# Kernel tuning notes

Measured on AMD Instinct MI355X. Metric: run time of the kernel, lower is better.

The kernel has to match this reference:

```python
import jax, jax.numpy as jnp
import numpy as np

B, S, D, H = 4, 1024, 1024, 16
HD = D // H          # head space dim = 64
FF = 4 * D           # ffn hidden = 4096
EPS = 1e-6

# ---- Lorentz manifold helpers (curvature k=1: -t^2 + |s|^2 = -1) ----

def to_manifold(space):
    t = jnp.sqrt(jnp.sum(space * space, -1, keepdims=True) + 1.0)
    return jnp.concatenate([t, space], -1)

def l_inner(x, y):
    return -x[..., 0] * y[..., 0] + jnp.sum(x[..., 1:] * y[..., 1:], -1)

def project(z):
    # renormalize onto hyperboloid: z / sqrt(|<z,z>_L|)   (Lorentz midpoint / LResNet)
    d = jnp.sqrt(jnp.clip(-l_inner(z, z), EPS))
    return z / d[..., None]

def hyp_layernorm(x, g, b):
    s = x[..., 1:]
    mu = jnp.mean(s, -1, keepdims=True)
    var = jnp.var(s, -1, keepdims=True)
    s = (s - mu) * jax.lax.rsqrt(var + 1e-5) * g + b
    return to_manifold(s)

def apply_rope(xs, cos, sin):
    # xs [B,S,H,HD]; cos/sin [S,HD//2]; freqs broadcast as [1,S,1,HD//2]
    x2 = xs.reshape(*xs.shape[:-1], HD // 2, 2)
    c = cos[None, :, None, :]
    s = sin[None, :, None, :]
    xr = x2[..., 0] * c - x2[..., 1] * s
    xi = x2[..., 0] * s + x2[..., 1] * c
    return jnp.stack([xr, xi], -1).reshape(xs.shape)


def setup_inputs() -> dict:
    key = jax.random.key(0)
    ks = jax.random.split(key, 8)
    def w(k, shape, fan_in):
        return jax.random.normal(k, shape, jnp.float32) / np.sqrt(fan_in).astype(np.float32)
    x = to_manifold(0.5 * jax.random.normal(ks[0], (B, S, D), jnp.float32))
    pos = jnp.arange(S, dtype=jnp.float32)[:, None]
    inv = 1.0 / (10000.0 ** (jnp.arange(0, HD, 2, dtype=jnp.float32) / HD))
    ang = pos * inv[None, :]
    return {
        'x': x,
        'rope_cos': jnp.cos(ang), 'rope_sin': jnp.sin(ang),
        'norm1_g': jnp.ones((D,), jnp.float32), 'norm1_b': jnp.zeros((D,), jnp.float32),
        'Wq': w(ks[1], (H, D + 1, HD), D + 1), 'bq': jnp.zeros((H, HD), jnp.float32),
        'Wk': w(ks[2], (H, D + 1, HD), D + 1), 'bk': jnp.zeros((H, HD), jnp.float32),
        'Wv': w(ks[3], (H, D + 1, HD), D + 1), 'bv': jnp.zeros((H, HD), jnp.float32),
        'attn_scale': jnp.asarray(np.sqrt(HD), jnp.float32),
        'attn_bias': jnp.zeros((), jnp.float32),
        'Wo': w(ks[4], (H * (HD + 1), D), H * (HD + 1)), 'bo': jnp.zeros((D,), jnp.float32),
        'w_res1': jnp.asarray(1.0, jnp.float32),
        'norm2_g': jnp.ones((D,), jnp.float32), 'norm2_b': jnp.zeros((D,), jnp.float32),
        'W1': w(ks[5], (D + 1, FF), D + 1), 'b1': jnp.zeros((FF,), jnp.float32),
        'W2': w(ks[6], (FF + 1, D), FF + 1), 'b2': jnp.zeros((D,), jnp.float32),
        'w_res2': jnp.asarray(1.0, jnp.float32),
    }


def reference(x, rope_cos, rope_sin, norm1_g, norm1_b, Wq, bq, Wk, bk, Wv, bv,
              attn_scale, attn_bias, Wo, bo, w_res1, norm2_g, norm2_b,
              W1, b1, W2, b2, w_res2):
    # ---- pre-norm ----
    xn = hyp_layernorm(x, norm1_g, norm1_b)
    # ---- per-head Lorentz linear (space part), inline RoPE on q/k ----
    qs = jnp.einsum('bsd,hde->bshe', xn, Wq) + bq          # [B,S,H,HD]
    ksp = jnp.einsum('bsd,hde->bshe', xn, Wk) + bk
    vsp = jnp.einsum('bsd,hde->bshe', xn, Wv) + bv
    qs = apply_rope(qs, rope_cos, rope_sin)
    ksp = apply_rope(ksp, rope_cos, rope_sin)
    # hyperbolic normalization of q/k: unit space norm, time recomputed
    qs = qs * jax.lax.rsqrt(jnp.sum(qs * qs, -1, keepdims=True) + EPS)
    ksp = ksp * jax.lax.rsqrt(jnp.sum(ksp * ksp, -1, keepdims=True) + EPS)
    q = to_manifold(qs)                                    # [B,S,H,HD+1]
    k = to_manifold(ksp)
    v = to_manifold(vsp)
    # ---- curvature-aware scores: 2 + 2 <q,k>_L (neg sq Lorentz distance) ----
    sgn = jnp.concatenate([-jnp.ones((1,), q.dtype), jnp.ones((HD,), q.dtype)])
    cin = jnp.einsum('bshe,bthe->bhst', q * sgn, k)        # Minkowski inner [B,H,S,S]
    att = (2.0 + 2.0 * cin) / attn_scale + attn_bias
    P = jax.nn.softmax(att, axis=-1)
    # ---- Lorentz midpoint aggregation of values ----
    m = jnp.einsum('bhst,bthe->bshe', P, v)
    m = project(m)                                         # back onto hyperboloid
    # ---- heads concat + output Lorentz linear ----
    cat = m.reshape(B, S, H * (HD + 1))
    attn_out = to_manifold(cat @ Wo + bo)
    # ---- LResNet residual 1 ----
    x = project(x + w_res1 * attn_out)
    # ---- Lorentz FFN ----
    h = hyp_layernorm(x, norm2_g, norm2_b)
    h = to_manifold(jax.nn.gelu(h @ W1 + b1))
    mlp = to_manifold(h @ W2 + b2)
    # ---- LResNet residual 2 ----
    x = project(x + w_res2 * mlp)
    return x
```

## Files before the change

kernel.cpp:

```cpp
#include <hip/hip_runtime.h>
#include <hip/hip_bf16.h>

typedef __hip_bfloat16 bf16;
typedef __attribute__((ext_vector_type(8))) short short8;
typedef __attribute__((ext_vector_type(4))) float f32x4;

#define B_  4
#define S_  1024
#define H_  16
#define R_  4096
#define LD_ 1088

#define MBL 1048576L
#define OFF_WQKVT (0L)
#define OFF_WOT   (6684672L)
#define OFF_X2    (0L)
#define OFF_W1T   (9L*MBL)
#define OFF_W2T   (18L*MBL)
#define OFF_BIAS  (26L*MBL)
#define OFF_XNB   (27L*MBL + MBL/2)
#define OFF_MCAT  OFF_XNB
#define OFF_HBUF  OFF_XNB
#define OFF_QPS   (36L*MBL)
#define OFF_ARAW  OFF_QPS
#define OFF_KPS   (44L*MBL)
#define OFF_VT    (52L*MBL)
#define OFF_QT    (62L*MBL)
#define OFF_KT    (62L*MBL + 262144L)
#define OFF_HHBIG (44L*MBL)
#define OFF_MLPB  (76L*MBL)
#define OFF_HHC   (36L*MBL)
#define OFF_MLPF  (44L*MBL)
#define BQKV 0
#define BOF  16384
#define B1F  32768
#define B2F  65536
#define W2R0 81920
#define RCF  98304
#define RSNF 262144
#define SCLF 409600
#define TACC 425984
#define FLAG 458752

__device__ __forceinline__ bf16  f2bf(float v) { return __float2bfloat16(v); }
__device__ __forceinline__ float bf2f(bf16 v)  { return __bfloat162float(v); }
__device__ __forceinline__ unsigned short bf2s(float v) {
  return __builtin_bit_cast(unsigned short, __float2bfloat16(v));
}
__device__ __forceinline__ float ldu(const void* p, long i, int isbf) {
  return isbf ? bf2f(((const bf16*)p)[i]) : ((const float*)p)[i];
}
__device__ __forceinline__ void stu(void* p, long i, float v, int isbf) {
  if (isbf) ((bf16*)p)[i] = f2bf(v);
  else      ((float*)p)[i] = v;
}
__device__ __forceinline__ float gelu_f(float v) {
  const float u = 0.7978845608028654f * (v + 0.044715f * v * v * v);
  const float e = __expf(fminf(2.f * u, 80.f));
  return 0.5f * v * (1.f + (e - 1.f) / (e + 1.f));
}
__device__ __forceinline__ float bfu_lo(unsigned u) {
  return __builtin_bit_cast(float, u << 16);
}
__device__ __forceinline__ float bfu_hi(unsigned u) {
  return __builtin_bit_cast(float, u & 0xFFFF0000u);
}

__device__ __forceinline__ void gload16(const bf16* g, short* l) {
  __builtin_amdgcn_global_load_lds(
      (const __attribute__((address_space(1))) unsigned int*)g,
      (__attribute__((address_space(3))) unsigned int*)l, 16, 0, 0);
}

__global__ void detect_kernel(const unsigned* __restrict__ g, int* __restrict__ flag) {
  if (threadIdx.x == 0) flag[0] = (g[0] == 0x3F803F80u) ? 1 : 0;
}

__global__ __launch_bounds__(256) void zero16_kernel(uint4* __restrict__ p, int n16) {
  int i = blockIdx.x * 256 + threadIdx.x;
  if (i < n16) p[i] = uint4{0, 0, 0, 0};
}

__device__ __forceinline__ float bred_f(float v, float* sh) {
#pragma unroll
  for (int o = 32; o; o >>= 1) v += __shfl_xor(v, o);
  __syncthreads();
  if ((threadIdx.x & 63) == 0) sh[threadIdx.x >> 6] = v;
  __syncthreads();
  return sh[0] + sh[1] + sh[2] + sh[3];
}
__device__ __forceinline__ double bred_d(double v, double* sh) {
#pragma unroll
  for (int o = 32; o; o >>= 1) v += __shfl_xor(v, o);
  __syncthreads();
  if ((threadIdx.x & 63) == 0) sh[threadIdx.x >> 6] = v;
  __syncthreads();
  return sh[0] + sh[1] + sh[2] + sh[3];
}

__global__ __launch_bounds__(256) void mega_prep(
    const void* x, const void* rc, const void* rsn, const void* n1g, const void* n1b,
    const void* Wq, const void* bq, const void* Wk, const void* bk,
    const void* Wv, const void* bv, const void* scl, const void* ab,
    const void* Wo, const void* bo, const void* wr1,
    const void* W1, const void* b1, const void* W2, const void* b2, const void* wr2,
    char* bias_base, bf16* __restrict__ wqkvT, bf16* __restrict__ woT,
    bf16* __restrict__ w1T, bf16* __restrict__ w2T, bf16* __restrict__ xnb,
    const int* __restrict__ flag) {
  const int isbf = flag[0];
  __shared__ float tl[64][65];
  const int tid = threadIdx.x;
  int bid = blockIdx.x;
  if (bid < 297) {
    int i = bid * 256 + tid;
    float* bqkvf = (float*)(bias_base + BQKV);
    if (i < 1024)        { bqkvf[i] = ldu(bq, i, isbf); return; }
    if (i < 2048)        { bqkvf[i] = ldu(bk, i - 1024, isbf); return; }
    if (i < 3072)        { bqkvf[i] = ldu(bv, i - 2048, isbf); return; }
    if (i < 4096)        { ((float*)(bias_base + BOF))[i - 3072] = ldu(bo, i - 3072, isbf); return; }
    if (i < 8192)        { ((float*)(bias_base + B1F))[i - 4096] = ldu(b1, i - 4096, isbf); return; }
    if (i < 9216)        { ((float*)(bias_base + B2F))[i - 8192] = ldu(b2, i - 8192, isbf); return; }
    if (i < 10240)       { ((float*)(bias_base + W2R0))[i - 9216] = ldu(W2, i - 9216, isbf); return; }
    if (i < 10240+32768) { ((float*)(bias_base + RCF))[i - 10240] = ldu(rc, i - 10240, isbf); return; }
    if (i < 10240+65536) { ((float*)(bias_base + RSNF))[i - 43008] = ldu(rsn, i - 43008, isbf); return; }
    if (i == 75776)      { ((float*)(bias_base + SCLF))[0] = ldu(scl, 0, isbf); return; }
    if (i == 75777)      { ((float*)(bias_base + SCLF))[1] = ldu(ab, 0, isbf); return; }
    if (i == 75778)      { ((float*)(bias_base + SCLF))[2] = ldu(wr1, 0, isbf); return; }
    if (i == 75779)      { ((float*)(bias_base + SCLF))[3] = ldu(wr2, 0, isbf); return; }
    return;
  }
  bid -= 297;
  const int tx = tid & 63, tg = tid >> 6;
  if (bid < 816) {
    int k0 = (bid % 17) * 64, z = bid / 17;
    int mode = z >> 4, h = z & 15;
    const void* src = (mode == 0) ? Wq : (mode == 1) ? Wk : Wv;
    const long soff = (long)h * 1025 * 64;
    int base_n = mode * 1024 + h * 64;
    for (int i = tg; i < 64; i += 4) {
      int k = k0 + i;
      tl[i][tx] = (k < 1025) ? ldu(src, soff + (long)k * 64 + tx, isbf) : 0.f;
    }
    __syncthreads();
    for (int i = tg; i < 64; i += 4) {
      int k = k0 + tx;
      if (k < LD_) wqkvT[(long)(base_n + i) * LD_ + k] = f2bf(tl[tx][i]);
    }
    return;
  }
  bid -= 816;
  if (bid < 272) {
    int k0 = (bid % 17) * 64, n0 = (bid / 17) * 64;
    for (int i = tg; i < 64; i += 4) {
      int kp = k0 + i;
      float v = 0.f;
      if (kp < 1056) {
        int h = kp / 66, e = kp - h * 66;
        if (e < 65) v = ldu(Wo, (long)(h * 65 + e) * 1024 + n0 + tx, isbf);
      }
      tl[i][tx] = v;
    }
    __syncthreads();
    for (int i = tg; i < 64; i += 4) {
      int kp = k0 + tx;
      if (kp < LD_) woT[(long)(n0 + i) * LD_ + kp] = f2bf(tl[tx][i]);
    }
    return;
  }
  bid -= 272;
  if (bid < 1088) {
    int k0 = (bid % 17) * 64, n0 = (bid / 17) * 64;
    for (int i = tg; i < 64; i += 4) {
      int k = k0 + i;
      tl[i][tx] = (k < 1025) ? ldu(W1, (long)k * 4096 + n0 + tx, isbf) : 0.f;
    }
    __syncthreads();
    for (int i = tg; i < 64; i += 4) {
      int k = k0 + tx;
      if (k < LD_) w1T[(long)(n0 + i) * LD_ + k] = f2bf(tl[tx][i]);
    }
    return;
  }
  bid -= 1088;
  if (bid < 1024) {
    int k0 = (bid % 64) * 64, n0 = (bid / 64) * 64;
    for (int i = tg; i < 64; i += 4) {
      int k = k0 + i;
      tl[i][tx] = ldu(W2, 1024 + (long)k * 1024 + n0 + tx, isbf);
    }
    __syncthreads();
    for (int i = tg; i < 64; i += 4) {
      int k = k0 + tx;
      w2T[(long)(n0 + i) * 4096 + k] = f2bf(tl[tx][i]);
    }
    return;
  }
  bid -= 1024;
  {
    float* red = &tl[0][0];
    const long base = (long)bid * 1025;
    const long obase = (long)bid * LD_;
    float v[4];
#pragma unroll
    for (int i = 0; i < 4; i++) v[i] = ldu(x, base + 1 + tid * 4 + i, isbf);
    float s = 0.f, s2 = 0.f;
#pragma unroll
    for (int i = 0; i < 4; i++) { s += v[i]; s2 += v[i] * v[i]; }
    s  = bred_f(s,  red);
    s2 = bred_f(s2, red);
    const float mu  = s * (1.f / 1024.f);
    const float var = s2 * (1.f / 1024.f) - mu * mu;
    const float rs  = rsqrtf(var + 1e-5f);
    float n[4], ns = 0.f;
#pragma unroll
    for (int i = 0; i < 4; i++) {
      const int e = tid * 4 + i;
      n[i] = (v[i] - mu) * rs * ldu(n1g, e, isbf) + ldu(n1b, e, isbf);
      ns += n[i] * n[i];
    }
    ns = bred_f(ns, red);
    if (tid == 0) xnb[obase] = f2bf(sqrtf(ns + 1.f));
#pragma unroll
    for (int i = 0; i < 4; i++) xnb[obase + 1 + tid * 4 + i] = f2bf(n[i]);
    if (tid < 63) xnb[obase + 1025 + tid] = f2bf(0.f);
  }
}

template <int EPI, bool SS>
__global__ __launch_bounds__(256) void mfma_gemm(const bf16* __restrict__ A, int lda,
                                                 const bf16* __restrict__ Bw, int ldb, int K,
                                                 const float* __restrict__ bias,
                                                 void* __restrict__ Cv, int ldc, int accf,
                                                 float* __restrict__ tacc) {
  __shared__ __align__(16) short As[2][128 * 32];
  __shared__ __align__(16) short Bs[2][64 * 32];
  const int tid = threadIdx.x, lane = tid & 63, wv = tid >> 6;
  const int quad = lane >> 4, q15 = lane & 15;
  const int wave_m = wv & 1, wave_n = wv >> 1;
  const int n0 = blockIdx.x * 64, m0 = blockIdx.y * 128;
  const int sa0 = wv * 128 + lane, sa1 = sa0 + 64;
  const int ra0 = sa0 >> 2, ca0 = (sa0 & 3) ^ (ra0 & 3);
  const int ra1 = sa1 >> 2, ca1 = (sa1 & 3) ^ (ra1 & 3);
  const int rb = tid >> 2, cb = (tid & 3) ^ (rb & 3);
  const int kswz = (quad ^ (q15 & 3)) * 8;
  const bf16* pa0 = A + (long)(m0 + ra0) * lda + ca0 * 8;
  const bf16* pa1 = A + (long)(m0 + ra1) * lda + ca1 * 8;
  const bf16* pb  = Bw + (long)(n0 + rb) * ldb + cb * 8;
  f32x4 acc[4][2] = {};
  for (int k0 = 0; k0 < K; k0 += 64) {
#pragma unroll
    for (int p = 0; p < 2; p++) {
      gload16(pa0 + p * 32, As[p] + sa0 * 8);
      gload16(pa1 + p * 32, As[p] + sa1 * 8);
      gload16(pb + p * 32, Bs[p] + tid * 8);
    }
    pa0 += 64; pa1 += 64; pb += 64;
    __syncthreads();
#pragma unroll
    for (int p = 0; p < 2; p++) {
      short8 af[4], bfr[2];
#pragma unroll
      for (int i = 0; i < 4; i++)
        af[i] = *(const short8*)(As[p] + (wave_m * 64 + i * 16 + q15) * 32 + kswz);
#pragma unroll
      for (int i = 0; i < 2; i++)
        bfr[i] = *(const short8*)(Bs[p] + (wave_n * 32 + i * 16 + q15) * 32 + kswz);
#pragma unroll
      for (int mi = 0; mi < 4; mi++)
#pragma unroll
        for (int ni = 0; ni < 2; ni++)
          acc[mi][ni] = __builtin_amdgcn_mfma_f32_16x16x32_bf16(af[mi], bfr[ni], acc[mi][ni], 0, 0, 0);
    }
    __syncthreads();
  }
#pragma unroll
  for (int mi = 0; mi < 4; mi++) {
#pragma unroll
    for (int r = 0; r < 4; r++) {
      const int m = m0 + wave_m * 64 + mi * 16 + quad * 4 + r;
      float s2 = 0.f;
#pragma unroll
      for (int ni = 0; ni < 2; ni++) {
        const int n = n0 + wave_n * 32 + ni * 16 + q15;
        float v = acc[mi][ni][r] + (bias ? bias[n] : 0.f);
        const long idx = (long)m * ldc + n;
        if (EPI == 0) {
          float* Cf = (float*)Cv;
          if (accf) v += Cf[idx];
          Cf[idx] = v;
        } else if (EPI == 1) {
          ((bf16*)Cv)[idx] = f2bf(v);
        } else {
          v = gelu_f(v);
          ((bf16*)Cv)[idx] = f2bf(v);
        }
        if (SS) s2 += v * v;
      }
      if (SS) {
        s2 += __shfl_xor(s2, 1);
        s2 += __shfl_xor(s2, 2);
        s2 += __shfl_xor(s2, 4);
        s2 += __shfl_xor(s2, 8);
        if (q15 == 0) atomicAdd(tacc + m, s2);
      }
    }
  }
}

template <int EPI>
__global__ __launch_bounds__(256) void mfma_gemm128(const bf16* __restrict__ A, int lda,
                                                    const bf16* __restrict__ Bw, int ldb, int K,
                                                    const float* __restrict__ bias,
                                                    void* __restrict__ Cv, int ldc, int accf) {
  __shared__ __align__(16) short As[2][128 * 32];
  __shared__ __align__(16) short Bs[2][128 * 32];
  const int tid = threadIdx.x, lane = tid & 63, wv = tid >> 6;
  const int quad = lane >> 4, q15 = lane & 15;
  const int wave_m = wv & 1, wave_n = wv >> 1;
  const int n0 = blockIdx.x * 128, m0 = blockIdx.y * 128;
  const int s0 = wv * 128 + lane, s1 = s0 + 64;
  const int r0 = s0 >> 2, c0 = (s0 & 3) ^ (r0 & 3);
  const int r1 = s1 >> 2, c1 = (s1 & 3) ^ (r1 & 3);
  const int kswz = (quad ^ (q15 & 3)) * 8;
  const bf16* pa0 = A + (long)(m0 + r0) * lda + c0 * 8;
  const bf16* pa1 = A + (long)(m0 + r1) * lda + c1 * 8;
  const bf16* pb0 = Bw + (long)(n0 + r0) * ldb + c0 * 8;
  const bf16* pb1 = Bw + (long)(n0 + r1) * ldb + c1 * 8;
  f32x4 acc[4][4] = {};
  for (int k0 = 0; k0 < K; k0 += 64) {
#pragma unroll
    for (int p = 0; p < 2; p++) {
      gload16(pa0 + p * 32, As[p] + s0 * 8);
      gload16(pa1 + p * 32, As[p] + s1 * 8);
      gload16(pb0 + p * 32, Bs[p] + s0 * 8);
      gload16(pb1 + p * 32, Bs[p] + s1 * 8);
    }
    pa0 += 64; pa1 += 64; pb0 += 64; pb1 += 64;
    __syncthreads();
#pragma unroll
    for (int p = 0; p < 2; p++) {
      short8 af[4], bfr[4];
#pragma unroll
      for (int i = 0; i < 4; i++) {
        af[i]  = *(const short8*)(As[p] + (wave_m * 64 + i * 16 + q15) * 32 + kswz);
        bfr[i] = *(const short8*)(Bs[p] + (wave_n * 64 + i * 16 + q15) * 32 + kswz);
      }
#pragma unroll
      for (int mi = 0; mi < 4; mi++)
#pragma unroll
        for (int ni = 0; ni < 4; ni++)
          acc[mi][ni] = __builtin_amdgcn_mfma_f32_16x16x32_bf16(af[mi], bfr[ni], acc[mi][ni], 0, 0, 0);
    }
    __syncthreads();
  }
#pragma unroll
  for (int mi = 0; mi < 4; mi++) {
#pragma unroll
    for (int r = 0; r < 4; r++) {
      const int m = m0 + wave_m * 64 + mi * 16 + quad * 4 + r;
#pragma unroll
      for (int ni = 0; ni < 4; ni++) {
        const int n = n0 + wave_n * 64 + ni * 16 + q15;
        float v = acc[mi][ni][r] + (bias ? bias[n] : 0.f);
        const long idx = (long)m * ldc + n;
        if (EPI == 0) {
          float* Cf = (float*)Cv;
          if (accf) v += Cf[idx];
          Cf[idx] = v;
        } else if (EPI == 1) {
          ((bf16*)Cv)[idx] = f2bf(v);
        } else {
          ((bf16*)Cv)[idx] = f2bf(gelu_f(v));
        }
      }
    }
  }
}

__global__ __launch_bounds__(256) void gemm_qkv(const bf16* __restrict__ A,
                                                const bf16* __restrict__ Wt,
                                                const char* __restrict__ bias_base,
                                                bf16* __restrict__ qPs, float* __restrict__ qtc,
                                                bf16* __restrict__ kPs, float* __restrict__ ktc,
                                                bf16* __restrict__ vT) {
  __shared__ __align__(16) short As[2][128 * 32];
  __shared__ __align__(16) short Bs[2][128 * 32];
  const int tid = threadIdx.x, lane = tid & 63, wv = tid >> 6;
  const int quad = lane >> 4, q15 = lane & 15;
  const int wave_m = wv & 1, wave_n = wv >> 1;
  const int n0 = blockIdx.x * 128, m0 = blockIdx.y * 128;
  const int s0 = wv * 128 + lane, s1 = s0 + 64;
  const int r0 = s0 >> 2, c0 = (s0 & 3) ^ (r0 & 3);
  const int r1 = s1 >> 2, c1 = (s1 & 3) ^ (r1 & 3);
  const int kswz = (quad ^ (q15 & 3)) * 8;
  const float* bqkvf = (const float*)(bias_base + BQKV);
  const float* rcf   = (const float*)(bias_base + RCF);
  const float* rsnf  = (const float*)(bias_base + RSNF);
  const bf16* pa0 = A + (long)(m0 + r0) * LD_ + c0 * 8;
  const bf16* pa1 = A + (long)(m0 + r1) * LD_ + c1 * 8;
  const bf16* pb0 = Wt + (long)(n0 + r0) * LD_ + c0 * 8;
  const bf16* pb1 = Wt + (long)(n0 + r1) * LD_ + c1 * 8;
  f32x4 acc[4][4] = {};
  for (int k0 = 0; k0 < LD_; k0 += 64) {
#pragma unroll
    for (int p = 0; p < 2; p++) {
      gload16(pa0 + p * 32, As[p] + s0 * 8);
      gload16(pa1 + p * 32, As[p] + s1 * 8);
      gload16(pb0 + p * 32, Bs[p] + s0 * 8);
      gload16(pb1 + p * 32, Bs[p] + s1 * 8);
    }
    pa0 += 64; pa1 += 64; pb0 += 64; pb1 += 64;
    __syncthreads();
#pragma unroll
    for (int p = 0; p < 2; p++) {
      short8 af[4], bfr[4];
#pragma unroll
      for (int i = 0; i < 4; i++) {
        af[i]  = *(const short8*)(As[p] + (wave_m * 64 + i * 16 + q15) * 32 + kswz);
        bfr[i] = *(const short8*)(Bs[p] + (wave_n * 64 + i * 16 + q15) * 32 + kswz);
      }
#pragma unroll
      for (int mi = 0; mi < 4; mi++)
#pragma unroll
        for (int ni = 0; ni < 4; ni++)
          acc[mi][ni] = __builtin_amdgcn_mfma_f32_16x16x32_bf16(af[mi], bfr[ni], acc[mi][ni], 0, 0, 0);
    }
    __syncthreads();
  }
  const int hg = (n0 >> 6) + wave_n;
  const int mode = hg >> 4, h = hg & 15;
  const int nb = hg * 64;
#pragma unroll
  for (int mi = 0; mi < 4; mi++) {
#pragma unroll
    for (int r = 0; r < 4; r++) {
      const int m = m0 + wave_m * 64 + mi * 16 + quad * 4 + r;
      const int bb = m >> 10, s = m & 1023;
      const int bh = bb * H_ + h;
      float v[4];
#pragma unroll
      for (int ns = 0; ns < 4; ns++) v[ns] = acc[mi][ns][r] + bqkvf[nb + ns * 16 + q15];
      if (mode < 2) {
#pragma unroll
        for (int ns = 0; ns < 4; ns++) {
          const int eg = ns * 16 + q15;
          const int j = eg >> 1;
          const float c = rcf[s * 32 + j], sn = rsnf[s * 32 + j];
          const float p = __shfl_xor(v[ns], 1);
          v[ns] = ((eg & 1) == 0) ? (v[ns] * c - p * sn) : (p * sn + v[ns] * c);
        }
      }
      float ss = v[0] * v[0] + v[1] * v[1] + v[2] * v[2] + v[3] * v[3];
#pragma unroll
      for (int o = 8; o; o >>= 1) ss += __shfl_xor(ss, o);
      if (mode == 0) {
        const float sc = rsqrtf(ss + 1e-6f);
        const long rb2 = (long)(bh * 1024 + s) * 64;
#pragma unroll
        for (int ns = 0; ns < 4; ns++) qPs[rb2 + ns * 16 + q15] = f2bf(v[ns] * sc);
        if (q15 == 0) qtc[bh * 1024 + s] = sqrtf(ss / (ss + 1e-6f) + 1.f);
      } else if (mode == 1) {
        const float sc = rsqrtf(ss + 1e-6f);
        const long rb2 = (long)(bh * 1024 + s) * 64;
#pragma unroll
        for (int ns = 0; ns < 4; ns++) kPs[rb2 + ns * 16 + q15] = f2bf(v[ns] * sc);
        if (q15 == 0) ktc[bh * 1024 + s] = sqrtf(ss / (ss + 1e-6f) + 1.f);
      } else {
        const long vb = (long)bh * 81920;
#pragma unroll
        for (int ns = 0; ns < 4; ns++) vT[vb + (long)(1 + ns * 16 + q15) * 1024 + s] = f2bf(v[ns]);
        if (q15 == 0) vT[vb + s] = f2bf(sqrtf(ss + 1.f));
      }
    }
  }
}

__global__ __launch_bounds__(256) void attn_kernel(const bf16* __restrict__ qPs,
                                                   const float* __restrict__ qtc,
                                                   const bf16* __restrict__ kPs,
                                                   const float* __restrict__ ktc,
                                                   const bf16* __restrict__ vT,
                                                   const float* __restrict__ scalf,
                                                   bf16* __restrict__ mcat) {
  __shared__ __align__(16) short kbuf[64 * 72];
  __shared__ __align__(16) short vbuf[80 * 72];
  __shared__ __align__(16) short pbuf[64 * 72];
  __shared__ float tkl[64];
  const int tid = threadIdx.x, lane = tid & 63, wv = tid >> 6;
  const int quad = lane >> 4, q15 = lane & 15;
  const int id = blockIdx.x;
  const int cxd = id & 7, jj_ = id >> 3;
  const int bh = cxd * 8 + (jj_ & 7), qt_ = jj_ >> 3;
  const float inv_scale = 1.f / scalf[0];
  const long qrow = (long)(bh * 1024 + qt_ * 64 + wv * 16 + q15) * 64;
  const short8 aq0 = *(const short8*)(qPs + qrow + quad * 8);
  const short8 aq1 = *(const short8*)(qPs + qrow + 32 + quad * 8);
  float tqr[4];
#pragma unroll
  for (int r = 0; r < 4; r++) tqr[r] = qtc[bh * 1024 + qt_ * 64 + wv * 16 + quad * 4 + r];
  f32x4 out[5];
#pragma unroll
  for (int mt = 0; mt < 5; mt++) out[mt] = f32x4{0, 0, 0, 0};
  float lip[4] = {0.f, 0.f, 0.f, 0.f};
  const int srcl = (q15 >> 2) << 4;
  for (int kt = 0; kt < 16; kt++) {
    __syncthreads();
#pragma unroll
    for (int c = 0; c < 2; c++) {
      const int id2 = c * 256 + tid, row = id2 >> 3, off = id2 & 7;
      *(uint4*)(kbuf + row * 72 + off * 8) =
          *(const uint4*)(kPs + (long)(bh * 1024 + kt * 64 + row) * 64 + off * 8);
    }
#pragma unroll
    for (int c = 0; c < 3; c++) {
      const int id2 = c * 256 + tid;
      if (id2 < 640) {
        const int row = id2 >> 3, off = id2 & 7;
        *(uint4*)(vbuf + row * 72 + off * 8) =
            *(const uint4*)(vT + (long)bh * 81920 + (long)row * 1024 + kt * 64 + off * 8);
      }
    }
    if (tid < 64) tkl[tid] = ktc[bh * 1024 + kt * 64 + tid];
    __syncthreads();
    f32x4 sacc[4] = {f32x4{0,0,0,0}, f32x4{0,0,0,0}, f32x4{0,0,0,0}, f32x4{0,0,0,0}};
#pragma unroll
    for (int ns = 0; ns < 4; ns++) {
      short8 b0 = *(const short8*)(kbuf + (ns * 16 + q15) * 72 + quad * 8);
      short8 b1 = *(const short8*)(kbuf + (ns * 16 + q15) * 72 + 32 + quad * 8);
      sacc[ns] = __builtin_amdgcn_mfma_f32_16x16x32_bf16(aq0, b0, sacc[ns], 0, 0, 0);
      sacc[ns] = __builtin_amdgcn_mfma_f32_16x16x32_bf16(aq1, b1, sacc[ns], 0, 0, 0);
    }
#pragma unroll
    for (int ns = 0; ns < 4; ns++) {
      const float tk = tkl[ns * 16 + q15];
#pragma unroll
      for (int r = 0; r < 4; r++) {
        const float pv = __expf((2.f + 2.f * (sacc[ns][r] - tqr[r] * tk)) * inv_scale);
        lip[r] += pv;
        pbuf[(wv * 16 + quad * 4 + r) * 72 + ns * 16 + q15] = (short)bf2s(pv);
      }
    }
#pragma unroll
    for (int mt = 0; mt < 5; mt++)
#pragma unroll
      for (int kc = 0; kc < 2; kc++) {
        short8 av = *(const short8*)(vbuf + (mt * 16 + q15) * 72 + kc * 32 + quad * 8);
        short8 bp = *(const short8*)(pbuf + (wv * 16 + q15) * 72 + kc * 32 + quad * 8);
        out[mt] = __builtin_amdgcn_mfma_f32_16x16x32_bf16(av, bp, out[mt], 0, 0, 0);
      }
  }
  {
#pragma unroll
    for (int o = 8; o; o >>= 1)
#pragma unroll
      for (int r = 0; r < 4; r++) lip[r] += __shfl_xor(lip[r], o);
    float linv[4];
#pragma unroll
    for (int r = 0; r < 4; r++) linv[r] = 1.f / lip[r];
    const float t0 = __shfl(linv[0], srcl), t1 = __shfl(linv[1], srcl);
    const float t2 = __shfl(linv[2], srcl), t3 = __shfl(linv[3], srcl);
    const int rr = q15 & 3;
    const float lv = (rr == 0) ? t0 : (rr == 1) ? t1 : (rr == 2) ? t2 : t3;
#pragma unroll
    for (int mt = 0; mt < 5; mt++)
#pragma unroll
      for (int j = 0; j < 4; j++) out[mt][j] *= lv;
  }
  float part = 0.f;
#pragma unroll
  for (int mt = 0; mt < 5; mt++)
#pragma unroll
    for (int j = 0; j < 4; j++) {
      const int e = mt * 16 + quad * 4 + j;
      const float vv = out[mt][j] * out[mt][j];
      part += (e == 0) ? vv : -vv;
    }
  part += __shfl_xor(part, 16);
  part += __shfl_xor(part, 32);
  const float dinv = rsqrtf(fmaxf(part, 1e-6f));
  __syncthreads();
  short* obuf = vbuf;
  const int qrow_l = wv * 16 + q15;
#pragma unroll
  for (int mt = 0; mt < 5; mt++)
#pragma unroll
    for (int j = 0; j < 4; j++) {
      const int e = mt * 16 + quad * 4 + j;
      if (e <= 64) obuf[qrow_l * 72 + e] = (short)bf2s(out[mt][j] * dinv);
    }
  if (quad == 1) obuf[qrow_l * 72 + 65] = 0;
  __syncthreads();
  const int b = bh >> 4, h = bh & 15;
  const long outbase = ((long)b * 1024 + qt_ * 64) * LD_ + h * 66;
  for (int i = tid; i < 64 * 33; i += 256) {
    const int row = i / 33, p = i - row * 33;
    *(unsigned*)(mcat + outbase + (long)row * LD_ + p * 2) =
        *(const unsigned*)(obuf + row * 72 + p * 2);
  }
  if (h == 15) {
    const long zb = ((long)b * 1024 + qt_ * 64) * LD_ + 1056;
    for (int i = tid; i < 64 * 16; i += 256) {
      const int row = i >> 4, p = i & 15;
      *(unsigned*)(mcat + zb + (long)row * LD_ + p * 2) = 0u;
    }
  }
}

__global__ __launch_bounds__(256) void final_fix_kernel(const float* __restrict__ t_acc,
                                                        const float* __restrict__ w2r0,
                                                        const float* __restrict__ b2f,
                                                        float* __restrict__ mlp) {
  const int m = blockIdx.x;
  const float t = sqrtf(1.f + t_acc[m]);
  float* row = mlp + (long)m * 1024;
  for (int n = threadIdx.x; n < 1024; n += 256) row[n] += t * w2r0[n] + b2f[n];
}

__global__ __launch_bounds__(256) void final_fix_big(const bf16* __restrict__ hh,
                                                     const float* __restrict__ w2r0,
                                                     const float* __restrict__ b2f,
                                                     float* __restrict__ mlp) {
  __shared__ float red[4];
  const int m = blockIdx.x;
  const uint4* r4 = (const uint4*)(hh + (long)m * 4096);
  float ss = 0.f;
  for (int i = threadIdx.x; i < 512; i += 256) {
    const uint4 u = r4[i];
    const unsigned a[4] = {u.x, u.y, u.z, u.w};
#pragma unroll
    for (int j = 0; j < 4; j++) {
      const float lo = bfu_lo(a[j]), hi = bfu_hi(a[j]);
      ss += lo * lo + hi * hi;
    }
  }
  ss = bred_f(ss, red);
  const float t = sqrtf(1.f + ss);
  float* row = mlp + (long)m * 1024;
  for (int n = threadIdx.x; n < 1024; n += 256) row[n] += t * w2r0[n] + b2f[n];
}

__global__ __launch_bounds__(256) void proj_ln_kernel(
    const void* __restrict__ x, const bf16* __restrict__ c,
    const float* __restrict__ scalf, int widx,
    const void* __restrict__ g, const void* __restrict__ b,
    bf16* __restrict__ x2, bf16* __restrict__ hbuf, const int* __restrict__ flag) {
  const int isbf = flag[0];
  __shared__ double redd[4];
  __shared__ float redf[4];
  const long bx = (long)blockIdx.x * 1025;
  const long bc = (long)blockIdx.x * 1024;
  const long ob = (long)blockIdx.x * LD_;
  const int tid = threadIdx.x;
  const double w = (double)scalf[widx];
  const float x0 = ldu(x, bx, isbf);
  float xs[4], cv[4];
#pragma unroll
  for (int i = 0; i < 4; i++) {
    xs[i] = ldu(x, bx + 1 + tid * 4 + i, isbf);
    cv[i] = bf2f(c[bc + tid * 4 + i]);
  }
  double cc = 0.0, xx = 0.0, xc = 0.0, sx = 0.0, sc_ = 0.0;
#pragma unroll
  for (int i = 0; i < 4; i++) {
    cc += (double)cv[i] * cv[i];
    xx += (double)xs[i] * xs[i];
    xc += (double)xs[i] * cv[i];
    sx += (double)xs[i];
    sc_ += (double)cv[i];
  }
  cc = bred_d(cc, redd);
  xx = bred_d(xx, redd);
  xc = bred_d(xc, redd);
  sx = bred_d(sx, redd);
  sc_ = bred_d(sc_, redd);
  const double t   = sqrt(1.0 + cc);
  const double lxx = (double)x0 * x0 - xx;
  const double xm  = -(double)x0 * t + xc;
  double d2 = lxx + w * w - 2.0 * w * xm;
  if (d2 < 1e-6) d2 = 1e-6;
  const double dinv = 1.0 / sqrt(d2);
  if (tid == 0) x2[bx] = f2bf((float)(((double)x0 + w * t) * dinv));
  float z[4];
#pragma unroll
  for (int i = 0; i < 4; i++) {
    z[i] = (float)(((double)xs[i] + w * cv[i]) * dinv);
    x2[bx + 1 + tid * 4 + i] = f2bf(z[i]);
  }
  const float sumz  = (float)((sx + w * sc_) * dinv);
  const float sumsq = (float)((xx + 2.0 * w * xc + w * w * cc) * dinv * dinv);
  const float mu  = sumz * (1.f / 1024.f);
  const float var = sumsq * (1.f / 1024.f) - mu * mu;
  const float rs  = rsqrtf(var + 1e-5f);
  float n[4], ns = 0.f;
#pragma unroll
  for (int i = 0; i < 4; i++) {
    const int e = tid * 4 + i;
    n[i] = (z[i] - mu) * rs * ldu(g, e, isbf) + ldu(b, e, isbf);
    ns += n[i] * n[i];
  }
  ns = bred_f(ns, redf);
  if (tid == 0) hbuf[ob] = f2bf(sqrtf(ns + 1.f));
#pragma unroll
  for (int i = 0; i < 4; i++) hbuf[ob + 1 + tid * 4 + i] = f2bf(n[i]);
  if (tid < 63) hbuf[ob + 1025 + tid] = f2bf(0.f);
}

__global__ __launch_bounds__(256) void res_project_kernel(
    const void* __restrict__ x, int xtag, const void* __restrict__ c, int ctag,
    const float* __restrict__ scalf, int widx, void* __restrict__ out, int otag,
    const int* __restrict__ flag) {
  const int isbf = flag[0];
  const int xb = (xtag == 2) ? isbf : xtag;
  const int cb2 = (ctag == 2) ? isbf : ctag;
  const int ob = (otag == 2) ? isbf : otag;
  __shared__ double red[4];
  const long bx = (long)blockIdx.x * 1025;
  const long bc = (long)blockIdx.x * 1024;
  const int tid = threadIdx.x;
  const double w = (double)scalf[widx];
  const float x0 = ldu(x, bx, xb);
  float xs[4], cv[4];
#pragma unroll
  for (int i = 0; i < 4; i++) {
    xs[i] = ldu(x, bx + 1 + tid * 4 + i, xb);
    cv[i] = ldu(c, bc + tid * 4 + i, cb2);
  }
  double cc = 0.0, xx = 0.0, xc = 0.0;
#pragma unroll
  for (int i = 0; i < 4; i++) {
    cc += (double)cv[i] * cv[i];
    xx += (double)xs[i] * xs[i];
    xc += (double)xs[i] * cv[i];
  }
  cc = bred_d(cc, red);
  xx = bred_d(xx, red);
  xc = bred_d(xc, red);
  const double t   = sqrt(1.0 + cc);
  const double lxx = (double)x0 * x0 - xx;
  const double xm  = -(double)x0 * t + xc;
  double d2 = lxx + w * w - 2.0 * w * xm;
  if (d2 < 1e-6) d2 = 1e-6;
  const double dinv = 1.0 / sqrt(d2);
  if (tid == 0) stu(out, bx, (float)(((double)x0 + w * t) * dinv), ob);
#pragma unroll
  for (int i = 0; i < 4; i++)
    stu(out, bx + 1 + tid * 4 + i, (float)(((double)xs[i] + w * cv[i]) * dinv), ob);
}

extern "C" void kernel_launch(void* const* d_in, const int* in_sizes, int n_in,
                              void* d_out, int out_size, void* d_ws, size_t ws_size,
                              hipStream_t stream) {
  char* w = (char*)d_ws;
  char* bias_base = w + OFF_BIAS;
  int* flag = (int*)(bias_base + FLAG);
  float* tacc = (float*)(bias_base + TACC);
  const float* scalf = (const float*)(bias_base + SCLF);
  const bool big = ws_size >= (size_t)92 * MBL;
  char* mlp_off = big ? (w + OFF_MLPB) : (w + OFF_MLPF);

  detect_kernel<<<1, 64, 0, stream>>>((const unsigned*)d_in[3], flag);
  zero16_kernel<<<4, 256, 0, stream>>>((uint4*)tacc, 1024);

  mega_prep<<<7593, 256, 0, stream>>>(
      d_in[0], d_in[1], d_in[2], d_in[3], d_in[4], d_in[5], d_in[6], d_in[7], d_in[8],
      d_in[9], d_in[10], d_in[11], d_in[12], d_in[13], d_in[14], d_in[15], d_in[18],
      d_in[19], d_in[20], d_in[21], d_in[22], bias_base, (bf16*)(w + OFF_WQKVT),
      (bf16*)(w + OFF_WOT), (bf16*)(w + OFF_W1T), (bf16*)(w + OFF_W2T),
      (bf16*)(w + OFF_XNB), flag);

  gemm_qkv<<<dim3(24, 32), 256, 0, stream>>>(
      (const bf16*)(w + OFF_XNB), (const bf16*)(w + OFF_WQKVT), bias_base,
      (bf16*)(w + OFF_QPS), (float*)(w + OFF_QT), (bf16*)(w + OFF_KPS),
      (float*)(w + OFF_KT), (bf16*)(w + OFF_VT));
  attn_kernel<<<1024, 256, 0, stream>>>(
      (const bf16*)(w + OFF_QPS), (const float*)(w + OFF_QT), (const bf16*)(w + OFF_KPS),
      (const float*)(w + OFF_KT), (const bf16*)(w + OFF_VT), scalf, (bf16*)(w + OFF_MCAT));
  mfma_gemm<1, false><<<dim3(16, 32), 256, 0, stream>>>(
      (const bf16*)(w + OFF_MCAT), LD_, (const bf16*)(w + OFF_WOT), LD_, LD_,
      (const float*)(bias_base + BOF), w + OFF_ARAW, 1024, 0, nullptr);
  proj_ln_kernel<<<R_, 256, 0, stream>>>(d_in[0], (const bf16*)(w + OFF_ARAW), scalf, 2,
                                         d_in[16], d_in[17], (bf16*)(w + OFF_X2),
                                         (bf16*)(w + OFF_HBUF), flag);
  if (big) {
    mfma_gemm128<2><<<dim3(32, 32), 256, 0, stream>>>(
        (const bf16*)(w + OFF_HBUF), LD_, (const bf16*)(w + OFF_W1T), LD_, LD_,
        (const float*)(bias_base + B1F), w + OFF_HHBIG, 4096, 0);
    mfma_gemm<0, false><<<dim3(16, 32), 256, 0, stream>>>(
        (const bf16*)(w + OFF_HHBIG), 4096, (const bf16*)(w + OFF_W2T), 4096, 4096,
        nullptr, mlp_off, 1024, 0, nullptr);
    final_fix_big<<<R_, 256, 0, stream>>>((const bf16*)(w + OFF_HHBIG),
                                          (const float*)(bias_base + W2R0),
                                          (const float*)(bias_base + B2F),
                                          (float*)mlp_off);
  } else {
    for (int c = 0; c < 4; c++) {
      mfma_gemm<2, true><<<dim3(16, 32), 256, 0, stream>>>(
          (const bf16*)(w + OFF_HBUF), LD_, (const bf16*)(w + OFF_W1T) + (long)c * 1024 * LD_,
          LD_, LD_, (const float*)(bias_base + B1F) + c * 1024, w + OFF_HHC, 1024, 0, tacc);
      mfma_gemm<0, false><<<dim3(16, 32), 256, 0, stream>>>(
          (const bf16*)(w + OFF_HHC), 1024, (const bf16*)(w + OFF_W2T) + c * 1024, 4096, 1024,
          nullptr, mlp_off, 1024, c > 0 ? 1 : 0, nullptr);
    }
    final_fix_kernel<<<R_, 256, 0, stream>>>(tacc, (const float*)(bias_base + W2R0),
                                             (const float*)(bias_base + B2F),
                                             (float*)mlp_off);
  }
  res_project_kernel<<<R_, 256, 0, stream>>>(w + OFF_X2, 1, mlp_off, 0, scalf, 3,
                                             d_out, 2, flag);
}
```

Before: 470.4 us.

## Replace QKV and FFN-up GEMMs with 256x256-tile, 8-wave, 4-stage pipelined kernel

Adds a shared gemm256 main loop that uses 256x256 output tiles, 512 threads and a 4-deep LDS ring with loads issued two stages ahead. It splits A/B prefetch between the two MFMA half-phases, using s_setprio and explicit vmcnt waits. The QKV projection (with its RoPE/normalize epilogue) and the W1+GELU GEMM now use it in place of the 128x128 double-buffered kernels. The goal is more data reuse per tile and overlap of global loads with MFMA work. The cost is 128KB of LDS per block and far fewer blocks (192 for QKV, 256 for W1), which risks poor occupancy and wave quantization across 256 CUs.

```diff
diff --git a/kernel.cpp b/kernel.cpp
--- a/kernel.cpp
+++ b/kernel.cpp
@@ -226,6 +226,183 @@
   }
 }
 
+__device__ __forceinline__ void gemm256_main(const bf16* __restrict__ A, int lda,
+                                             const bf16* __restrict__ Bw, int ldb, int K,
+                                             short (*__restrict__ As)[8192],
+                                             short (*__restrict__ Bs)[8192],
+                                             f32x4 (*acc)[4]) {
+  const int tid = threadIdx.x, lane = tid & 63, wv = tid >> 6;
+  const int quad = lane >> 4, q15 = lane & 15;
+  const int wave_m = wv >> 2, wave_n = wv & 3;
+  const int m0 = blockIdx.y * 256, n0 = blockIdx.x * 256;
+  const int NT = K >> 5;
+  const int u0 = tid, u1 = tid + 512;
+  const int r0 = u0 >> 2, c0 = ((u0 & 3) ^ ((u0 >> 3) & 3)) * 8;
+  const int r1 = u1 >> 2, c1 = ((u1 & 3) ^ ((u1 >> 3) & 3)) * 8;
+  const bf16* pa0 = A + (long)(m0 + r0) * lda + c0;
+  const bf16* pa1 = A + (long)(m0 + r1) * lda + c1;
+  const bf16* pb0 = Bw + (long)(n0 + r0) * ldb + c0;
+  const bf16* pb1 = Bw + (long)(n0 + r1) * ldb + c1;
+  const int d0 = u0 * 8, d1 = u1 * 8;
+  const int kswz = (quad ^ ((q15 >> 1) & 3)) * 8;
+  const int arow = wave_m * 128 + q15;
+  const int brow = wave_n * 64 + q15;
+  gload16(pa0, As[0] + d0); gload16(pa1, As[0] + d1);
+  gload16(pb0, Bs[0] + d0); gload16(pb1, Bs[0] + d1);
+  pa0 += 32; pa1 += 32; pb0 += 32; pb1 += 32;
+  gload16(pa0, As[1] + d0); gload16(pa1, As[1] + d1);
+  gload16(pb0, Bs[1] + d0); gload16(pb1, Bs[1] + d1);
+  pa0 += 32; pa1 += 32; pb0 += 32; pb1 += 32;
+  asm volatile("s_waitcnt vmcnt(4)" ::: "memory");
+  __builtin_amdgcn_s_barrier();
+#pragma unroll 1
+  for (int t = 0; t < NT; ++t) {
+    const int buf = t & 3, sb = (t + 2) & 3;
+    const short* ab = As[buf];
+    const short* bb = Bs[buf];
+    short8 af[4], bfr[4];
+#pragma unroll
+    for (int i = 0; i < 4; i++) {
+      af[i]  = *(const short8*)(ab + (arow + i * 16) * 32 + kswz);
+      bfr[i] = *(const short8*)(bb + (brow + i * 16) * 32 + kswz);
+    }
+    if (t + 2 < NT) {
+      gload16(pa0, As[sb] + d0); gload16(pa1, As[sb] + d1);
+      pa0 += 32; pa1 += 32;
+    }
+    __builtin_amdgcn_s_barrier();
+    __builtin_amdgcn_s_setprio(1);
+#pragma unroll
+    for (int mi = 0; mi < 4; mi++)
+#pragma unroll
+      for (int ni = 0; ni < 4; ni++)
+        acc[mi][ni] = __builtin_amdgcn_mfma_f32_16x16x32_bf16(af[mi], bfr[ni], acc[mi][ni], 0, 0, 0);
+    __builtin_amdgcn_s_setprio(0);
+    __builtin_amdgcn_s_barrier();
+#pragma unroll
+    for (int i = 0; i < 4; i++)
+      af[i] = *(const short8*)(ab + (arow + 64 + i * 16) * 32 + kswz);
+    if (t + 2 < NT) {
+      gload16(pb0, Bs[sb] + d0); gload16(pb1, Bs[sb] + d1);
+      pb0 += 32; pb1 += 32;
+      asm volatile("s_waitcnt vmcnt(4)" ::: "memory");
+    } else {
+      asm volatile("s_waitcnt vmcnt(0)" ::: "memory");
+    }
+    __builtin_amdgcn_s_barrier();
+    __builtin_amdgcn_s_setprio(1);
+#pragma unroll
+    for (int mi = 0; mi < 4; mi++)
+#pragma unroll
+      for (int ni = 0; ni < 4; ni++)
+        acc[4 + mi][ni] = __builtin_amdgcn_mfma_f32_16x16x32_bf16(af[mi], bfr[ni], acc[4 + mi][ni], 0, 0, 0);
+    __builtin_amdgcn_s_setprio(0);
+    __builtin_amdgcn_s_barrier();
+  }
+}
+
+template <int EPI>
+__global__ __launch_bounds__(512) void gemm256(const bf16* __restrict__ A, int lda,
+                                               const bf16* __restrict__ Bw, int ldb, int K,
+                                               const float* __restrict__ bias,
+                                               void* __restrict__ Cv, int ldc, int accf) {
+  __shared__ __align__(16) short As[4][8192];
+  __shared__ __align__(16) short Bs[4][8192];
+  f32x4 acc[8][4] = {};
+  gemm256_main(A, lda, Bw, ldb, K, As, Bs, acc);
+  const int tid = threadIdx.x, lane = tid & 63, wv = tid >> 6;
+  const int quad = lane >> 4, q15 = lane & 15;
+  const int wave_m = wv >> 2, wave_n = wv & 3;
+  const int m0 = blockIdx.y * 256, n0 = blockIdx.x * 256;
+#pragma unroll
+  for (int j = 0; j < 8; j++) {
+#pragma unroll
+    for (int r = 0; r < 4; r++) {
+      const int m = m0 + wave_m * 128 + (j >> 2) * 64 + (j & 3) * 16 + quad * 4 + r;
+#pragma unroll
+      for (int ni = 0; ni < 4; ni++) {
+        const int n = n0 + wave_n * 64 + ni * 16 + q15;
+        float v = acc[j][ni][r] + (bias ? bias[n] : 0.f);
+        const long idx = (long)m * ldc + n;
+        if (EPI == 0) {
+          float* Cf = (float*)Cv;
+          if (accf) v += Cf[idx];
+          Cf[idx] = v;
+        } else if (EPI == 1) {
+          ((bf16*)Cv)[idx] = f2bf(v);
+        } else {
+          ((bf16*)Cv)[idx] = f2bf(gelu_f(v));
+        }
+      }
+    }
+  }
+}
+
+__global__ __launch_bounds__(512) void gemm_qkv256(const bf16* __restrict__ A,
+                                                   const bf16* __restrict__ Wt,
+                                                   const char* __restrict__ bias_base,
+                                                   bf16* __restrict__ qPs, float* __restrict__ qtc,
+                                                   bf16* __restrict__ kPs, float* __restrict__ ktc,
+                                                   bf16* __restrict__ vT) {
+  __shared__ __align__(16) short As[4][8192];
+  __shared__ __align__(16) short Bs[4][8192];
+  f32x4 acc[8][4] = {};
+  gemm256_main(A, LD_, Wt, LD_, LD_, As, Bs, acc);
+  const int tid = threadIdx.x, lane = tid & 63, wv = tid >> 6;
+  const int quad = lane >> 4, q15 = lane & 15;
+  const int wave_m = wv >> 2, wave_n = wv & 3;
+  const int m0 = blockIdx.y * 256, n0 = blockIdx.x * 256;
+  const float* bqkvf = (const float*)(bias_base + BQKV);
+  const float* rcf   = (const float*)(bias_base + RCF);
+  const float* rsnf  = (const float*)(bias_base + RSNF);
+  const int hg = (n0 >> 6) + wave_n;
+  const int mode = hg >> 4, h = hg & 15;
+  const int nb = hg * 64;
+#pragma unroll
+  for (int j = 0; j < 8; j++) {
+#pragma unroll
+    for (int r = 0; r < 4; r++) {
+      const int m = m0 + wave_m * 128 + (j >> 2) * 64 + (j & 3) * 16 + quad * 4 + r;
+      const int bb = m >> 10, s = m & 1023;
+      const int bh = bb * H_ + h;
+      float v[4];
+#pragma unroll
+      for (int ns = 0; ns < 4; ns++) v[ns] = acc[j][ns][r] + bqkvf[nb + ns * 16 + q15];
+      if (mode < 2) {
+#pragma unroll
+        for (int ns = 0; ns < 4; ns++) {
+          const int eg = ns * 16 + q15;
+          const int jj = eg >> 1;
+          const float c = rcf[s * 32 + jj], sn = rsnf[s * 32 + jj];
+          const float p = __shfl_xor(v[ns], 1);
+          v[ns] = ((eg & 1) == 0) ? (v[ns] * c - p * sn) : (p * sn + v[ns] * c);
+        }
+      }
+      float ss = v[0] * v[0] + v[1] * v[1] + v[2] * v[2] + v[3] * v[3];
+#pragma unroll
+      for (int o = 8; o; o >>= 1) ss += __shfl_xor(ss, o);
+      if (mode == 0) {
+        const float sc = rsqrtf(ss + 1e-6f);
+        const long rb2 = (long)(bh * 1024 + s) * 64;
+#pragma unroll
+        for (int ns = 0; ns < 4; ns++) qPs[rb2 + ns * 16 + q15] = f2bf(v[ns] * sc);
+        if (q15 == 0) qtc[bh * 1024 + s] = sqrtf(ss / (ss + 1e-6f) + 1.f);
+      } else if (mode == 1) {
+        const float sc = rsqrtf(ss + 1e-6f);
+        const long rb2 = (long)(bh * 1024 + s) * 64;
+#pragma unroll
+        for (int ns = 0; ns < 4; ns++) kPs[rb2 + ns * 16 + q15] = f2bf(v[ns] * sc);
+        if (q15 == 0) ktc[bh * 1024 + s] = sqrtf(ss / (ss + 1e-6f) + 1.f);
+      } else {
+        const long vb = (long)bh * 81920;
+#pragma unroll
+        for (int ns = 0; ns < 4; ns++) vT[vb + (long)(1 + ns * 16 + q15) * 1024 + s] = f2bf(v[ns]);
+        if (q15 == 0) vT[vb + s] = f2bf(sqrtf(ss + 1.f));
+      }
+    }
+  }
+}
+
 template <int EPI, bool SS>
 __global__ __launch_bounds__(256) void mfma_gemm(const bf16* __restrict__ A, int lda,
                                                  const bf16* __restrict__ Bw, int ldb, int K,
@@ -307,174 +484,6 @@
   }
 }
 
-template <int EPI>
-__global__ __launch_bounds__(256) void mfma_gemm128(const bf16* __restrict__ A, int lda,
-                                                    const bf16* __restrict__ Bw, int ldb, int K,
-                                                    const float* __restrict__ bias,
-                                                    void* __restrict__ Cv, int ldc, int accf) {
-  __shared__ __align__(16) short As[2][128 * 32];
-  __shared__ __align__(16) short Bs[2][128 * 32];
-  const int tid = threadIdx.x, lane = tid & 63, wv = tid >> 6;
-  const int quad = lane >> 4, q15 = lane & 15;
-  const int wave_m = wv & 1, wave_n = wv >> 1;
-  const int n0 = blockIdx.x * 128, m0 = blockIdx.y * 128;
-  const int s0 = wv * 128 + lane, s1 = s0 + 64;
-  const int r0 = s0 >> 2, c0 = (s0 & 3) ^ (r0 & 3);
-  const int r1 = s1 >> 2, c1 = (s1 & 3) ^ (r1 & 3);
-  const int kswz = (quad ^ (q15 & 3)) * 8;
-  const bf16* pa0 = A + (long)(m0 + r0) * lda + c0 * 8;
-  const bf16* pa1 = A + (long)(m0 + r1) * lda + c1 * 8;
-  const bf16* pb0 = Bw + (long)(n0 + r0) * ldb + c0 * 8;
-  const bf16* pb1 = Bw + (long)(n0 + r1) * ldb + c1 * 8;
-  f32x4 acc[4][4] = {};
-  for (int k0 = 0; k0 < K; k0 += 64) {
-#pragma unroll
-    for (int p = 0; p < 2; p++) {
-      gload16(pa0 + p * 32, As[p] + s0 * 8);
-      gload16(pa1 + p * 32, As[p] + s1 * 8);
-      gload16(pb0 + p * 32, Bs[p] + s0 * 8);
-      gload16(pb1 + p * 32, Bs[p] + s1 * 8);
-    }
-    pa0 += 64; pa1 += 64; pb0 += 64; pb1 += 64;
-    __syncthreads();
-#pragma unroll
-    for (int p = 0; p < 2; p++) {
-      short8 af[4], bfr[4];
-#pragma unroll
-      for (int i = 0; i < 4; i++) {
-        af[i]  = *(const short8*)(As[p] + (wave_m * 64 + i * 16 + q15) * 32 + kswz);
-        bfr[i] = *(const short8*)(Bs[p] + (wave_n * 64 + i * 16 + q15) * 32 + kswz);
-      }
-#pragma unroll
-      for (int mi = 0; mi < 4; mi++)
-#pragma unroll
-        for (int ni = 0; ni < 4; ni++)
-          acc[mi][ni] = __builtin_amdgcn_mfma_f32_16x16x32_bf16(af[mi], bfr[ni], acc[mi][ni], 0, 0, 0);
-    }
-    __syncthreads();
-  }
-#pragma unroll
-  for (int mi = 0; mi < 4; mi++) {
-#pragma unroll
-    for (int r = 0; r < 4; r++) {
-      const int m = m0 + wave_m * 64 + mi * 16 + quad * 4 + r;
-#pragma unroll
-      for (int ni = 0; ni < 4; ni++) {
-        const int n = n0 + wave_n * 64 + ni * 16 + q15;
-        float v = acc[mi][ni][r] + (bias ? bias[n] : 0.f);
-        const long idx = (long)m * ldc + n;
-        if (EPI == 0) {
-          float* Cf = (float*)Cv;
-          if (accf) v += Cf[idx];
-          Cf[idx] = v;
-        } else if (EPI == 1) {
-          ((bf16*)Cv)[idx] = f2bf(v);
-        } else {
-          ((bf16*)Cv)[idx] = f2bf(gelu_f(v));
-        }
-      }
-    }
-  }
-}
-
-__global__ __launch_bounds__(256) void gemm_qkv(const bf16* __restrict__ A,
-                                                const bf16* __restrict__ Wt,
-                                                const char* __restrict__ bias_base,
-                                                bf16* __restrict__ qPs, float* __restrict__ qtc,
-                                                bf16* __restrict__ kPs, float* __restrict__ ktc,
-                                                bf16* __restrict__ vT) {
-  __shared__ __align__(16) short As[2][128 * 32];
-  __shared__ __align__(16) short Bs[2][128 * 32];
-  const int tid = threadIdx.x, lane = tid & 63, wv = tid >> 6;
-  const int quad = lane >> 4, q15 = lane & 15;
-  const int wave_m = wv & 1, wave_n = wv >> 1;
-  const int n0 = blockIdx.x * 128, m0 = blockIdx.y * 128;
-  const int s0 = wv * 128 + lane, s1 = s0 + 64;
-  const int r0 = s0 >> 2, c0 = (s0 & 3) ^ (r0 & 3);
-  const int r1 = s1 >> 2, c1 = (s1 & 3) ^ (r1 & 3);
-  const int kswz = (quad ^ (q15 & 3)) * 8;
-  const float* bqkvf = (const float*)(bias_base + BQKV);
-  const float* rcf   = (const float*)(bias_base + RCF);
-  const float* rsnf  = (const float*)(bias_base + RSNF);
-  const bf16* pa0 = A + (long)(m0 + r0) * LD_ + c0 * 8;
-  const bf16* pa1 = A + (long)(m0 + r1) * LD_ + c1 * 8;
-  const bf16* pb0 = Wt + (long)(n0 + r0) * LD_ + c0 * 8;
-  const bf16* pb1 = Wt + (long)(n0 + r1) * LD_ + c1 * 8;
-  f32x4 acc[4][4] = {};
-  for (int k0 = 0; k0 < LD_; k0 += 64) {
-#pragma unroll
-    for (int p = 0; p < 2; p++) {
-      gload16(pa0 + p * 32, As[p] + s0 * 8);
-      gload16(pa1 + p * 32, As[p] + s1 * 8);
-      gload16(pb0 + p * 32, Bs[p] + s0 * 8);
-      gload16(pb1 + p * 32, Bs[p] + s1 * 8);
-    }
-    pa0 += 64; pa1 += 64; pb0 += 64; pb1 += 64;
-    __syncthreads();
-#pragma unroll
-    for (int p = 0; p < 2; p++) {
-      short8 af[4], bfr[4];
-#pragma unroll
-      for (int i = 0; i < 4; i++) {
-        af[i]  = *(const short8*)(As[p] + (wave_m * 64 + i * 16 + q15) * 32 + kswz);
-        bfr[i] = *(const short8*)(Bs[p] + (wave_n * 64 + i * 16 + q15) * 32 + kswz);
-      }
-#pragma unroll
-      for (int mi = 0; mi < 4; mi++)
-#pragma unroll
-        for (int ni = 0; ni < 4; ni++)
-          acc[mi][ni] = __builtin_amdgcn_mfma_f32_16x16x32_bf16(af[mi], bfr[ni], acc[mi][ni], 0, 0, 0);
-    }
-    __syncthreads();
-  }
-  const int hg = (n0 >> 6) + wave_n;
-  const int mode = hg >> 4, h = hg & 15;
-  const int nb = hg * 64;
-#pragma unroll
-  for (int mi = 0; mi < 4; mi++) {
-#pragma unroll
-    for (int r = 0; r < 4; r++) {
-      const int m = m0 + wave_m * 64 + mi * 16 + quad * 4 + r;
-      const int bb = m >> 10, s = m & 1023;
-      const int bh = bb * H_ + h;
-      float v[4];
-#pragma unroll
-      for (int ns = 0; ns < 4; ns++) v[ns] = acc[mi][ns][r] + bqkvf[nb + ns * 16 + q15];
-      if (mode < 2) {
-#pragma unroll
-        for (int ns = 0; ns < 4; ns++) {
-          const int eg = ns * 16 + q15;
-          const int j = eg >> 1;
-          const float c = rcf[s * 32 + j], sn = rsnf[s * 32 + j];
-          const float p = __shfl_xor(v[ns], 1);
-          v[ns] = ((eg & 1) == 0) ? (v[ns] * c - p * sn) : (p * sn + v[ns] * c);
-        }
-      }
-      float ss = v[0] * v[0] + v[1] * v[1] + v[2] * v[2] + v[3] * v[3];
-#pragma unroll
-      for (int o = 8; o; o >>= 1) ss += __shfl_xor(ss, o);
-      if (mode == 0) {
-        const float sc = rsqrtf(ss + 1e-6f);
-        const long rb2 = (long)(bh * 1024 + s) * 64;
-#pragma unroll
-        for (int ns = 0; ns < 4; ns++) qPs[rb2 + ns * 16 + q15] = f2bf(v[ns] * sc);
-        if (q15 == 0) qtc[bh * 1024 + s] = sqrtf(ss / (ss + 1e-6f) + 1.f);
-      } else if (mode == 1) {
-        const float sc = rsqrtf(ss + 1e-6f);
-        const long rb2 = (long)(bh * 1024 + s) * 64;
-#pragma unroll
-        for (int ns = 0; ns < 4; ns++) kPs[rb2 + ns * 16 + q15] = f2bf(v[ns] * sc);
-        if (q15 == 0) ktc[bh * 1024 + s] = sqrtf(ss / (ss + 1e-6f) + 1.f);
-      } else {
-        const long vb = (long)bh * 81920;
-#pragma unroll
-        for (int ns = 0; ns < 4; ns++) vT[vb + (long)(1 + ns * 16 + q15) * 1024 + s] = f2bf(v[ns]);
-        if (q15 == 0) vT[vb + s] = f2bf(sqrtf(ss + 1.f));
-      }
-    }
-  }
-}
-
 __global__ __launch_bounds__(256) void attn_kernel(const bf16* __restrict__ qPs,
                                                    const float* __restrict__ qtc,
                                                    const bf16* __restrict__ kPs,
@@ -768,7 +777,7 @@
       (bf16*)(w + OFF_WOT), (bf16*)(w + OFF_W1T), (bf16*)(w + OFF_W2T),
       (bf16*)(w + OFF_XNB), flag);
 
-  gemm_qkv<<<dim3(24, 32), 256, 0, stream>>>(
+  gemm_qkv256<<<dim3(12, 16), 512, 0, stream>>>(
       (const bf16*)(w + OFF_XNB), (const bf16*)(w + OFF_WQKVT), bias_base,
       (bf16*)(w + OFF_QPS), (float*)(w + OFF_QT), (bf16*)(w + OFF_KPS),
       (float*)(w + OFF_KT), (bf16*)(w + OFF_VT));
@@ -782,7 +791,7 @@
                                          d_in[16], d_in[17], (bf16*)(w + OFF_X2),
                                          (bf16*)(w + OFF_HBUF), flag);
   if (big) {
-    mfma_gemm128<2><<<dim3(32, 32), 256, 0, stream>>>(
+    gemm256<2><<<dim3(16, 16), 512, 0, stream>>>(
         (const bf16*)(w + OFF_HBUF), LD_, (const bf16*)(w + OFF_W1T), LD_, LD_,
         (const float*)(bias_base + B1F), w + OFF_HHBIG, 4096, 0);
     mfma_gemm<0, false><<<dim3(16, 32), 256, 0, stream>>>(
```

After: 479.1 us. About the same (+1.8%).
